# Kernel tuning notes

Measured on AMD Instinct MI355X. Metric: run time of the kernel, lower is better.

Reference implementation:

```python
import jax, jax.numpy as jnp
import numpy as np

EMBED_DIM = 1024
NUM_HEADS = 16
HEAD_DIM = EMBED_DIM // NUM_HEADS


def setup_inputs() -> dict:
    key = jax.random.key(0)
    k1, k2, k3, k4, k5 = jax.random.split(key, 5)
    B, L, C = 4, 4096, EMBED_DIM
    s = 1.0 / np.sqrt(C)
    return {
        "x": jax.random.normal(k1, (B, L, C), dtype=jnp.float32),
        "qkv_w": jax.random.normal(k2, (3 * C, C), dtype=jnp.float32) * s,
        "qkv_b": jax.random.normal(k3, (3 * C,), dtype=jnp.float32) * 0.01,
        "out_w": jax.random.normal(k4, (C, C), dtype=jnp.float32) * s,
        "out_b": jax.random.normal(k5, (C,), dtype=jnp.float32) * 0.01,
        "num_frames": 16,
    }


def reference(x, qkv_w, qkv_b, out_w, out_b, num_frames):
    B, L, C = x.shape
    P = L // num_frames  # patches per frame
    H, D = NUM_HEADS, HEAD_DIM
    xf = x.reshape(B * num_frames, P, C)
    # fused QKV projection (torch Linear: y = x @ W^T + b)
    qkv = xf @ qkv_w.T + qkv_b                      # [BF, P, 3C]
    qkv = qkv.reshape(B * num_frames, P, 3, H, D)
    qkv = jnp.transpose(qkv, (2, 0, 3, 1, 4))        # [3, BF, H, P, D]
    q, k, v = qkv[0], qkv[1], qkv[2]
    scores = jnp.einsum("bhqd,bhkd->bhqk", q, k) / np.sqrt(D)
    attn = jax.nn.softmax(scores, axis=-1)
    out = jnp.einsum("bhqk,bhkd->bhqd", attn, v)     # [BF, H, P, D]
    out = jnp.transpose(out, (0, 2, 1, 3)).reshape(B, L, C)
    return out @ out_w.T + out_b
```

## Files before the change

### kernel.cpp

```cpp
#include <hip/hip_runtime.h>


typedef __bf16 bf16x8 __attribute__((ext_vector_type(8)));
typedef float f32x4 __attribute__((ext_vector_type(4)));

__device__ __forceinline__ void gload_lds16(const void* g, void* l) {
  __builtin_amdgcn_global_load_lds(
      (__attribute__((address_space(1))) void*)(g),
      (__attribute__((address_space(3))) void*)(l), 16, 0, 0);
}

__global__ __launch_bounds__(256) void cvt_f32_bf16(
    const float* __restrict__ in, __bf16* __restrict__ out, int n8) {
  int i = blockIdx.x * 256 + threadIdx.x;
  if (i >= n8) return;
  const float4* p = (const float4*)in;
  float4 a = p[2 * i];
  float4 b = p[2 * i + 1];
  bf16x8 v;
  v[0] = (__bf16)a.x; v[1] = (__bf16)a.y; v[2] = (__bf16)a.z; v[3] = (__bf16)a.w;
  v[4] = (__bf16)b.x; v[5] = (__bf16)b.y; v[6] = (__bf16)b.z; v[7] = (__bf16)b.w;
  ((bf16x8*)out)[i] = v;
}

template <bool BF16_OUT>
__global__ __launch_bounds__(256, 2) void gemm_bt(
    const __bf16* __restrict__ A, const __bf16* __restrict__ Bm,
    const float* __restrict__ bias, void* __restrict__ Cv,
    int M, int N, int K) {
  __shared__ alignas(16) __bf16 As[128 * 32];
  __shared__ alignas(16) __bf16 Bs[128 * 32];

  const int tid = threadIdx.x, lane = tid & 63, wid = tid >> 6;
  const int wm = wid >> 1, wn = wid & 1;
  const int bm = blockIdx.y, bn = blockIdx.x;

  f32x4 acc[4][4] = {};

  const int seg0 = wid * 64 + lane, seg1 = seg0 + 256;
  const __bf16* gA0 = A + (size_t)(bm * 128 + (seg0 >> 2)) * K + (seg0 & 3) * 8;
  const __bf16* gA1 = A + (size_t)(bm * 128 + (seg1 >> 2)) * K + (seg1 & 3) * 8;
  const __bf16* gB0 = Bm + (size_t)(bn * 128 + (seg0 >> 2)) * K + (seg0 & 3) * 8;
  const __bf16* gB1 = Bm + (size_t)(bn * 128 + (seg1 >> 2)) * K + (seg1 & 3) * 8;
  __bf16* lA0 = &As[seg0 * 8];
  __bf16* lA1 = &As[seg1 * 8];
  __bf16* lB0 = &Bs[seg0 * 8];
  __bf16* lB1 = &Bs[seg1 * 8];

  const int ar = lane & 15, kc = (lane >> 4) * 8;
  const __bf16* rA = &As[(wm * 64 + ar) * 32 + kc];
  const __bf16* rB = &Bs[(wn * 64 + ar) * 32 + kc];

  for (int k0 = 0; k0 < K; k0 += 32) {
    gload_lds16(gA0, lA0);
    gload_lds16(gA1, lA1);
    gload_lds16(gB0, lB0);
    gload_lds16(gB1, lB1);
    gA0 += 32; gA1 += 32; gB0 += 32; gB1 += 32;
    __syncthreads();
    bf16x8 av[4], bv[4];
#pragma unroll
    for (int m = 0; m < 4; ++m) av[m] = *(const bf16x8*)(rA + m * 16 * 32);
#pragma unroll
    for (int n = 0; n < 4; ++n) bv[n] = *(const bf16x8*)(rB + n * 16 * 32);
#pragma unroll
    for (int m = 0; m < 4; ++m)
#pragma unroll
      for (int n = 0; n < 4; ++n)
        acc[m][n] = __builtin_amdgcn_mfma_f32_16x16x32_bf16(av[m], bv[n],
                                                            acc[m][n], 0, 0, 0);
    __syncthreads();
  }

  const int r0 = (lane >> 4) * 4, c0 = lane & 15;
#pragma unroll
  for (int m = 0; m < 4; ++m) {
#pragma unroll
    for (int n = 0; n < 4; ++n) {
      int row = bm * 128 + wm * 64 + m * 16 + r0;
      int col = bn * 128 + wn * 64 + n * 16 + c0;
      float bb = bias[col];
#pragma unroll
      for (int r = 0; r < 4; ++r) {
        float v = acc[m][n][r] + bb;
        if (BF16_OUT)
          ((__bf16*)Cv)[(size_t)(row + r) * N + col] = (__bf16)v;
        else
          ((float*)Cv)[(size_t)(row + r) * N + col] = v;
      }
    }
  }
}

__global__ __launch_bounds__(256, 2) void attn_kernel(
    const __bf16* __restrict__ qkv, __bf16* __restrict__ attnOut) {
  __shared__ alignas(16) __bf16 Ks[256 * 64];
  __shared__ alignas(16) __bf16 Vt[64 * 256];
  __shared__ alignas(16) __bf16 Pl[4][64 * 32];

  const int h = blockIdx.x, bf = blockIdx.y;
  const int tid = threadIdx.x, lane = tid & 63, wid = tid >> 6;
  const int l15 = lane & 15, l4 = lane >> 4;

  const __bf16* base = qkv + (size_t)(bf * 256) * 3072 + h * 64;

#pragma unroll
  for (int rr = 0; rr < 8; ++rr) {
    int s = rr * 256 + wid * 64 + lane;
    int r = s >> 3, t = s & 7, c8 = t ^ (r & 7);
    gload_lds16(base + 1024 + (size_t)r * 3072 + c8 * 8, &Ks[s * 8]);
  }

  {
    const __bf16* vrow = base + 2048 + (size_t)tid * 3072;
    bf16x8 vv[8];
#pragma unroll
    for (int b8 = 0; b8 < 8; ++b8) vv[b8] = *(const bf16x8*)(vrow + b8 * 8);
#pragma unroll
    for (int b8 = 0; b8 < 8; ++b8)
#pragma unroll
      for (int e = 0; e < 8; ++e) {
        int d = b8 * 8 + e;
        Vt[d * 256 + (((tid >> 3) ^ (d & 7)) * 8) + (tid & 7)] = vv[b8][e];
      }
  }

  bf16x8 aq[4][2];
  const __bf16* qbase = base + (size_t)(wid * 64) * 3072;
#pragma unroll
  for (int m = 0; m < 4; ++m)
#pragma unroll
    for (int kk = 0; kk < 2; ++kk)
      aq[m][kk] =
          *(const bf16x8*)(qbase + (size_t)(m * 16 + l15) * 3072 + kk * 32 + l4 * 8);

  __syncthreads();

  float m_run[4][4], l_run[4][4];
#pragma unroll
  for (int m = 0; m < 4; ++m)
#pragma unroll
    for (int r = 0; r < 4; ++r) { m_run[m][r] = -3.0e38f; l_run[m][r] = 0.f; }
  f32x4 o[4][4] = {};

  __bf16* Pw = &Pl[wid][0];

  for (int jt = 0; jt < 8; ++jt) {
    f32x4 s[4][2] = {};
#pragma unroll
    for (int kk = 0; kk < 2; ++kk) {
      bf16x8 bk[2];
#pragma unroll
      for (int n = 0; n < 2; ++n) {
        int j = jt * 32 + n * 16 + l15;
        int c8 = kk * 4 + l4;
        bk[n] = *(const bf16x8*)&Ks[(j * 8 + (c8 ^ (j & 7))) * 8];
      }
#pragma unroll
      for (int m = 0; m < 4; ++m)
#pragma unroll
        for (int n = 0; n < 2; ++n)
          s[m][n] = __builtin_amdgcn_mfma_f32_16x16x32_bf16(aq[m][kk], bk[n],
                                                            s[m][n], 0, 0, 0);
    }
#pragma unroll
    for (int m = 0; m < 4; ++m)
#pragma unroll
      for (int r = 0; r < 4; ++r) {
        float a0 = s[m][0][r] * 0.125f, a1 = s[m][1][r] * 0.125f;
        float t = fmaxf(a0, a1);
        t = fmaxf(t, __shfl_xor(t, 1));
        t = fmaxf(t, __shfl_xor(t, 2));
        t = fmaxf(t, __shfl_xor(t, 4));
        t = fmaxf(t, __shfl_xor(t, 8));
        float mn = fmaxf(m_run[m][r], t);
        float al = __expf(m_run[m][r] - mn);
        m_run[m][r] = mn;
        float p0 = __expf(a0 - mn), p1 = __expf(a1 - mn);
        s[m][0][r] = p0; s[m][1][r] = p1;
        float rs = p0 + p1;
        rs += __shfl_xor(rs, 1);
        rs += __shfl_xor(rs, 2);
        rs += __shfl_xor(rs, 4);
        rs += __shfl_xor(rs, 8);
        l_run[m][r] = l_run[m][r] * al + rs;
#pragma unroll
        for (int nd = 0; nd < 4; ++nd) o[m][nd][r] *= al;
      }
#pragma unroll
    for (int m = 0; m < 4; ++m)
#pragma unroll
      for (int n = 0; n < 2; ++n)
#pragma unroll
        for (int r = 0; r < 4; ++r) {
          int q = m * 16 + l4 * 4 + r;
          int j = n * 16 + l15;
          Pw[q * 32 + (((j >> 3) ^ (q & 3)) * 8) + (j & 7)] = (__bf16)s[m][n][r];
        }
    bf16x8 ap[4];
#pragma unroll
    for (int m = 0; m < 4; ++m) {
      int q = m * 16 + l15;
      ap[m] = *(const bf16x8*)&Pw[q * 32 + ((l4 ^ (q & 3)) * 8)];
    }
    bf16x8 bv[4];
#pragma unroll
    for (int nd = 0; nd < 4; ++nd) {
      int d = nd * 16 + l15;
      int jb = jt * 4 + l4;
      bv[nd] = *(const bf16x8*)&Vt[d * 256 + ((jb ^ (d & 7)) * 8)];
    }
#pragma unroll
    for (int m = 0; m < 4; ++m)
#pragma unroll
      for (int nd = 0; nd < 4; ++nd)
        o[m][nd] = __builtin_amdgcn_mfma_f32_16x16x32_bf16(ap[m], bv[nd],
                                                           o[m][nd], 0, 0, 0);
  }

  __bf16* ob = attnOut + (size_t)(bf * 256 + wid * 64) * 1024 + h * 64;
#pragma unroll
  for (int m = 0; m < 4; ++m)
#pragma unroll
    for (int r = 0; r < 4; ++r) {
      float inv = 1.0f / l_run[m][r];
#pragma unroll
      for (int nd = 0; nd < 4; ++nd)
        ob[(size_t)(m * 16 + l4 * 4 + r) * 1024 + nd * 16 + l15] =
            (__bf16)(o[m][nd][r] * inv);
    }
}

extern "C" void kernel_launch(void* const* d_in, const int* in_sizes, int n_in,
                              void* d_out, int out_size, void* d_ws,
                              size_t ws_size, hipStream_t stream) {
  const float* x = (const float*)d_in[0];
  const float* qkv_w = (const float*)d_in[1];
  const float* qkv_b = (const float*)d_in[2];
  const float* out_w = (const float*)d_in[3];
  const float* out_b = (const float*)d_in[4];
  float* out = (float*)d_out;

  __bf16* xb = (__bf16*)d_ws;
  __bf16* qkvwb = xb + 16777216;
  __bf16* outwb = qkvwb + 3145728;
  __bf16* qkvb = outwb + 1048576;
  __bf16* attnb = qkvb + (size_t)16384 * 3072;

  cvt_f32_bf16<<<8192, 256, 0, stream>>>(x, xb, 16777216 / 8);
  cvt_f32_bf16<<<1536, 256, 0, stream>>>(qkv_w, qkvwb, 3145728 / 8);
  cvt_f32_bf16<<<512, 256, 0, stream>>>(out_w, outwb, 1048576 / 8);

  gemm_bt<true><<<dim3(24, 128), 256, 0, stream>>>(xb, qkvwb, qkv_b, qkvb,
                                                   16384, 3072, 1024);

  attn_kernel<<<dim3(16, 64), 256, 0, stream>>>(qkvb, attnb);

  gemm_bt<false><<<dim3(8, 128), 256, 0, stream>>>(attnb, outwb, out_b, out,
                                                   16384, 1024, 1024);
}
```

Baseline: 411.8 us.

## Replace GEMM with 256x256-tile double-buffered LDS kernel and XCD-aware block swizzle

Both projection GEMMs move from a single-buffered 128x128x32 tile with 4 waves to a 256x256x64 tile with 8 waves. Operand tiles are double-buffered in LDS through direct global-to-LDS loads with an XOR swizzle, and fine-grained vmcnt/barrier waits overlap the next tile's loads with MFMA work. Block IDs are remapped across the 8 XCDs, and s_setprio raises priority around the MFMA bursts. The larger tile raises arithmetic intensity, but it uses 128KB of LDS and many accumulator registers, which limits occupancy to one block per CU and leaves fewer blocks for the smaller output GEMM.

```diff
diff --git a/kernel.cpp b/kernel.cpp
--- a/kernel.cpp
+++ b/kernel.cpp
@@ -24,61 +24,154 @@
 }
 
 template <bool BF16_OUT>
-__global__ __launch_bounds__(256, 2) void gemm_bt(
+__global__ __launch_bounds__(512, 2) void gemm256(
     const __bf16* __restrict__ A, const __bf16* __restrict__ Bm,
     const float* __restrict__ bias, void* __restrict__ Cv,
     int M, int N, int K) {
-  __shared__ alignas(16) __bf16 As[128 * 32];
-  __shared__ alignas(16) __bf16 Bs[128 * 32];
+  __shared__ alignas(16) __bf16 Al[2][256 * 64];
+  __shared__ alignas(16) __bf16 Bl[2][256 * 64];
 
   const int tid = threadIdx.x, lane = tid & 63, wid = tid >> 6;
-  const int wm = wid >> 1, wn = wid & 1;
-  const int bm = blockIdx.y, bn = blockIdx.x;
-
-  f32x4 acc[4][4] = {};
-
-  const int seg0 = wid * 64 + lane, seg1 = seg0 + 256;
-  const __bf16* gA0 = A + (size_t)(bm * 128 + (seg0 >> 2)) * K + (seg0 & 3) * 8;
-  const __bf16* gA1 = A + (size_t)(bm * 128 + (seg1 >> 2)) * K + (seg1 & 3) * 8;
-  const __bf16* gB0 = Bm + (size_t)(bn * 128 + (seg0 >> 2)) * K + (seg0 & 3) * 8;
-  const __bf16* gB1 = Bm + (size_t)(bn * 128 + (seg1 >> 2)) * K + (seg1 & 3) * 8;
-  __bf16* lA0 = &As[seg0 * 8];
-  __bf16* lA1 = &As[seg1 * 8];
-  __bf16* lB0 = &Bs[seg0 * 8];
-  __bf16* lB1 = &Bs[seg1 * 8];
-
-  const int ar = lane & 15, kc = (lane >> 4) * 8;
-  const __bf16* rA = &As[(wm * 64 + ar) * 32 + kc];
-  const __bf16* rB = &Bs[(wn * 64 + ar) * 32 + kc];
-
-  for (int k0 = 0; k0 < K; k0 += 32) {
-    gload_lds16(gA0, lA0);
-    gload_lds16(gA1, lA1);
-    gload_lds16(gB0, lB0);
-    gload_lds16(gB1, lB1);
-    gA0 += 32; gA1 += 32; gB0 += 32; gB1 += 32;
-    __syncthreads();
-    bf16x8 av[4], bv[4];
-#pragma unroll
-    for (int m = 0; m < 4; ++m) av[m] = *(const bf16x8*)(rA + m * 16 * 32);
-#pragma unroll
-    for (int n = 0; n < 4; ++n) bv[n] = *(const bf16x8*)(rB + n * 16 * 32);
-#pragma unroll
-    for (int m = 0; m < 4; ++m)
-#pragma unroll
-      for (int n = 0; n < 4; ++n)
-        acc[m][n] = __builtin_amdgcn_mfma_f32_16x16x32_bf16(av[m], bv[n],
-                                                            acc[m][n], 0, 0, 0);
-    __syncthreads();
-  }
-
-  const int r0 = (lane >> 4) * 4, c0 = lane & 15;
-#pragma unroll
-  for (int m = 0; m < 4; ++m) {
-#pragma unroll
-    for (int n = 0; n < 4; ++n) {
-      int row = bm * 128 + wm * 64 + m * 16 + r0;
-      int col = bn * 128 + wn * 64 + n * 16 + c0;
+  const int wr = wid >> 2, wc = wid & 3;
+  const int l15 = lane & 15, l4 = lane >> 4;
+
+  const int nwg = gridDim.x * gridDim.y;
+  const int bid = blockIdx.y * gridDim.x + blockIdx.x;
+  const int q = nwg >> 3;
+  const int swz = (bid & 7) * q + (bid >> 3);
+  const int bn = swz % gridDim.x, bm = swz / gridDim.x;
+
+  const int NT = K >> 6;
+
+  const __bf16* gA[4];
+  const __bf16* gB[4];
+#pragma unroll
+  for (int c = 0; c < 4; ++c) {
+    int seg = c * 512 + tid;
+    int row = seg >> 3, bl = (seg & 7) ^ (row & 7);
+    gA[c] = A + (size_t)(bm * 256 + row) * K + bl * 8;
+    gB[c] = Bm + (size_t)(bn * 256 + row) * K + bl * 8;
+  }
+
+#define STAGE(b)                                         \
+  {                                                      \
+    _Pragma("unroll") for (int c = 0; c < 4; ++c) {      \
+      gload_lds16(gA[c], &Al[b][(c * 512 + tid) * 8]);   \
+      gA[c] += 64;                                       \
+    }                                                    \
+    _Pragma("unroll") for (int c = 0; c < 4; ++c) {      \
+      gload_lds16(gB[c], &Bl[b][(c * 512 + tid) * 8]);   \
+      gB[c] += 64;                                       \
+    }                                                    \
+  }
+
+  const int rsw = l15 & 7;
+  const int pk0 = ((l4) ^ rsw) * 8;
+  const int pk1 = ((4 + l4) ^ rsw) * 8;
+  const int aRow = (wr * 128 + l15) * 64;
+  const int bRow = (wc * 64 + l15) * 64;
+
+  f32x4 acc[8][4] = {};
+
+  STAGE(0);
+  STAGE(1);
+  asm volatile("s_waitcnt vmcnt(8)" ::: "memory");
+  __builtin_amdgcn_s_barrier();
+
+  for (int t = 0; t < NT; ++t) {
+    const __bf16* Ab = &Al[t & 1][0];
+    const __bf16* Bb = &Bl[t & 1][0];
+    const bool hasStage = (t + 2 < NT);
+    const bool hasNext = (t + 1 < NT);
+
+    bf16x8 b0 = *(const bf16x8*)(Bb + bRow + 0 * 1024 + pk0);
+    bf16x8 b1 = *(const bf16x8*)(Bb + bRow + 1 * 1024 + pk0);
+    bf16x8 b2 = *(const bf16x8*)(Bb + bRow + 2 * 1024 + pk0);
+    bf16x8 b3 = *(const bf16x8*)(Bb + bRow + 3 * 1024 + pk0);
+    bf16x8 x0 = *(const bf16x8*)(Ab + aRow + 0 * 1024 + pk0);
+    bf16x8 x1 = *(const bf16x8*)(Ab + aRow + 1 * 1024 + pk0);
+    bf16x8 x2 = *(const bf16x8*)(Ab + aRow + 2 * 1024 + pk0);
+    bf16x8 x3 = *(const bf16x8*)(Ab + aRow + 3 * 1024 + pk0);
+    __builtin_amdgcn_s_setprio(1);
+#pragma unroll
+    for (int n = 0; n < 4; ++n) {
+      bf16x8 bb = n == 0 ? b0 : n == 1 ? b1 : n == 2 ? b2 : b3;
+      acc[0][n] = __builtin_amdgcn_mfma_f32_16x16x32_bf16(x0, bb, acc[0][n], 0, 0, 0);
+      acc[1][n] = __builtin_amdgcn_mfma_f32_16x16x32_bf16(x1, bb, acc[1][n], 0, 0, 0);
+      acc[2][n] = __builtin_amdgcn_mfma_f32_16x16x32_bf16(x2, bb, acc[2][n], 0, 0, 0);
+      acc[3][n] = __builtin_amdgcn_mfma_f32_16x16x32_bf16(x3, bb, acc[3][n], 0, 0, 0);
+    }
+    __builtin_amdgcn_s_setprio(0);
+
+    x0 = *(const bf16x8*)(Ab + aRow + 4 * 1024 + pk0);
+    x1 = *(const bf16x8*)(Ab + aRow + 5 * 1024 + pk0);
+    x2 = *(const bf16x8*)(Ab + aRow + 6 * 1024 + pk0);
+    x3 = *(const bf16x8*)(Ab + aRow + 7 * 1024 + pk0);
+    __builtin_amdgcn_s_setprio(1);
+#pragma unroll
+    for (int n = 0; n < 4; ++n) {
+      bf16x8 bb = n == 0 ? b0 : n == 1 ? b1 : n == 2 ? b2 : b3;
+      acc[4][n] = __builtin_amdgcn_mfma_f32_16x16x32_bf16(x0, bb, acc[4][n], 0, 0, 0);
+      acc[5][n] = __builtin_amdgcn_mfma_f32_16x16x32_bf16(x1, bb, acc[5][n], 0, 0, 0);
+      acc[6][n] = __builtin_amdgcn_mfma_f32_16x16x32_bf16(x2, bb, acc[6][n], 0, 0, 0);
+      acc[7][n] = __builtin_amdgcn_mfma_f32_16x16x32_bf16(x3, bb, acc[7][n], 0, 0, 0);
+    }
+    __builtin_amdgcn_s_setprio(0);
+
+    b0 = *(const bf16x8*)(Bb + bRow + 0 * 1024 + pk1);
+    b1 = *(const bf16x8*)(Bb + bRow + 1 * 1024 + pk1);
+    b2 = *(const bf16x8*)(Bb + bRow + 2 * 1024 + pk1);
+    b3 = *(const bf16x8*)(Bb + bRow + 3 * 1024 + pk1);
+    x0 = *(const bf16x8*)(Ab + aRow + 0 * 1024 + pk1);
+    x1 = *(const bf16x8*)(Ab + aRow + 1 * 1024 + pk1);
+    x2 = *(const bf16x8*)(Ab + aRow + 2 * 1024 + pk1);
+    x3 = *(const bf16x8*)(Ab + aRow + 3 * 1024 + pk1);
+    __builtin_amdgcn_s_setprio(1);
+#pragma unroll
+    for (int n = 0; n < 4; ++n) {
+      bf16x8 bb = n == 0 ? b0 : n == 1 ? b1 : n == 2 ? b2 : b3;
+      acc[0][n] = __builtin_amdgcn_mfma_f32_16x16x32_bf16(x0, bb, acc[0][n], 0, 0, 0);
+      acc[1][n] = __builtin_amdgcn_mfma_f32_16x16x32_bf16(x1, bb, acc[1][n], 0, 0, 0);
+      acc[2][n] = __builtin_amdgcn_mfma_f32_16x16x32_bf16(x2, bb, acc[2][n], 0, 0, 0);
+      acc[3][n] = __builtin_amdgcn_mfma_f32_16x16x32_bf16(x3, bb, acc[3][n], 0, 0, 0);
+    }
+    __builtin_amdgcn_s_setprio(0);
+
+    x0 = *(const bf16x8*)(Ab + aRow + 4 * 1024 + pk1);
+    x1 = *(const bf16x8*)(Ab + aRow + 5 * 1024 + pk1);
+    x2 = *(const bf16x8*)(Ab + aRow + 6 * 1024 + pk1);
+    x3 = *(const bf16x8*)(Ab + aRow + 7 * 1024 + pk1);
+    asm volatile("s_waitcnt lgkmcnt(0)" ::: "memory");
+    __builtin_amdgcn_sched_barrier(0);
+    __builtin_amdgcn_s_barrier();
+    if (hasStage) STAGE(t & 1);
+    __builtin_amdgcn_s_setprio(1);
+#pragma unroll
+    for (int n = 0; n < 4; ++n) {
+      bf16x8 bb = n == 0 ? b0 : n == 1 ? b1 : n == 2 ? b2 : b3;
+      acc[4][n] = __builtin_amdgcn_mfma_f32_16x16x32_bf16(x0, bb, acc[4][n], 0, 0, 0);
+      acc[5][n] = __builtin_amdgcn_mfma_f32_16x16x32_bf16(x1, bb, acc[5][n], 0, 0, 0);
+      acc[6][n] = __builtin_amdgcn_mfma_f32_16x16x32_bf16(x2, bb, acc[6][n], 0, 0, 0);
+      acc[7][n] = __builtin_amdgcn_mfma_f32_16x16x32_bf16(x3, bb, acc[7][n], 0, 0, 0);
+    }
+    __builtin_amdgcn_s_setprio(0);
+    if (hasNext) {
+      if (hasStage)
+        asm volatile("s_waitcnt vmcnt(8)" ::: "memory");
+      else
+        asm volatile("s_waitcnt vmcnt(0)" ::: "memory");
+      __builtin_amdgcn_s_barrier();
+    }
+  }
+#undef STAGE
+
+  const int r0 = l4 * 4;
+#pragma unroll
+  for (int m = 0; m < 8; ++m) {
+#pragma unroll
+    for (int n = 0; n < 4; ++n) {
+      int row = bm * 256 + wr * 128 + m * 16 + r0;
+      int col = bn * 256 + wc * 64 + n * 16 + l15;
       float bb = bias[col];
 #pragma unroll
       for (int r = 0; r < 4; ++r) {
@@ -251,11 +344,11 @@
   cvt_f32_bf16<<<1536, 256, 0, stream>>>(qkv_w, qkvwb, 3145728 / 8);
   cvt_f32_bf16<<<512, 256, 0, stream>>>(out_w, outwb, 1048576 / 8);
 
-  gemm_bt<true><<<dim3(24, 128), 256, 0, stream>>>(xb, qkvwb, qkv_b, qkvb,
-                                                   16384, 3072, 1024);
+  gemm256<true><<<dim3(12, 64), 512, 0, stream>>>(xb, qkvwb, qkv_b, qkvb,
+                                                  16384, 3072, 1024);
 
   attn_kernel<<<dim3(16, 64), 256, 0, stream>>>(qkvb, attnb);
 
-  gemm_bt<false><<<dim3(8, 128), 256, 0, stream>>>(attnb, outwb, out_b, out,
-                                                   16384, 1024, 1024);
-}
+  gemm256<false><<<dim3(4, 64), 512, 0, stream>>>(attnb, outwb, out_b, out,
+                                                  16384, 1024, 1024);
+}
```

New measurement: 379.1 us. -7.9%, faster.

## Replace GEMM with 256x256 tile, multi-buffered LDS pipeline and XCD-aware block swizzle

Applied to the files above, without the earlier changes.

Replaces the 128x128 single-buffered GEMM with a 512-thread 256x256 tile kernel. Global-to-LDS loads for later K-steps are issued ahead of time into four LDS stages, with explicit vmcnt waits, barriers and raised scheduling priority around the MFMA bursts. It also remaps block IDs so neighbouring tiles land on the same XCD for better L2 reuse, and XOR-swizzles the LDS layout to avoid bank conflicts. The aim is to hide load latency and raise MFMA utilisation, at the cost of 128 KB of LDS per block and lower occupancy, with the hand-tuned wait counts fragile if the load pattern changes.

```diff
diff --git a/kernel.cpp b/kernel.cpp
--- a/kernel.cpp
+++ b/kernel.cpp
@@ -9,6 +9,8 @@
       (__attribute__((address_space(1))) void*)(g),
       (__attribute__((address_space(3))) void*)(l), 16, 0, 0);
 }
+
+#define VMW(N) asm volatile("s_waitcnt vmcnt(" #N ")" ::: "memory")
 
 __global__ __launch_bounds__(256) void cvt_f32_bf16(
     const float* __restrict__ in, __bf16* __restrict__ out, int n8) {
@@ -24,61 +26,105 @@
 }
 
 template <bool BF16_OUT>
-__global__ __launch_bounds__(256, 2) void gemm_bt(
+__global__ __launch_bounds__(512, 2) void gemm256(
     const __bf16* __restrict__ A, const __bf16* __restrict__ Bm,
     const float* __restrict__ bias, void* __restrict__ Cv,
     int M, int N, int K) {
-  __shared__ alignas(16) __bf16 As[128 * 32];
-  __shared__ alignas(16) __bf16 Bs[128 * 32];
+  __shared__ alignas(16) __bf16 Asl[2][2][256 * 32];
+  __shared__ alignas(16) __bf16 Bsl[2][2][256 * 32];
 
   const int tid = threadIdx.x, lane = tid & 63, wid = tid >> 6;
-  const int wm = wid >> 1, wn = wid & 1;
-  const int bm = blockIdx.y, bn = blockIdx.x;
-
-  f32x4 acc[4][4] = {};
-
-  const int seg0 = wid * 64 + lane, seg1 = seg0 + 256;
-  const __bf16* gA0 = A + (size_t)(bm * 128 + (seg0 >> 2)) * K + (seg0 & 3) * 8;
-  const __bf16* gA1 = A + (size_t)(bm * 128 + (seg1 >> 2)) * K + (seg1 & 3) * 8;
-  const __bf16* gB0 = Bm + (size_t)(bn * 128 + (seg0 >> 2)) * K + (seg0 & 3) * 8;
-  const __bf16* gB1 = Bm + (size_t)(bn * 128 + (seg1 >> 2)) * K + (seg1 & 3) * 8;
-  __bf16* lA0 = &As[seg0 * 8];
-  __bf16* lA1 = &As[seg1 * 8];
-  __bf16* lB0 = &Bs[seg0 * 8];
-  __bf16* lB1 = &Bs[seg1 * 8];
-
-  const int ar = lane & 15, kc = (lane >> 4) * 8;
-  const __bf16* rA = &As[(wm * 64 + ar) * 32 + kc];
-  const __bf16* rB = &Bs[(wn * 64 + ar) * 32 + kc];
-
-  for (int k0 = 0; k0 < K; k0 += 32) {
-    gload_lds16(gA0, lA0);
-    gload_lds16(gA1, lA1);
-    gload_lds16(gB0, lB0);
-    gload_lds16(gB1, lB1);
-    gA0 += 32; gA1 += 32; gB0 += 32; gB1 += 32;
-    __syncthreads();
-    bf16x8 av[4], bv[4];
-#pragma unroll
-    for (int m = 0; m < 4; ++m) av[m] = *(const bf16x8*)(rA + m * 16 * 32);
-#pragma unroll
-    for (int n = 0; n < 4; ++n) bv[n] = *(const bf16x8*)(rB + n * 16 * 32);
-#pragma unroll
-    for (int m = 0; m < 4; ++m)
-#pragma unroll
-      for (int n = 0; n < 4; ++n)
-        acc[m][n] = __builtin_amdgcn_mfma_f32_16x16x32_bf16(av[m], bv[n],
-                                                            acc[m][n], 0, 0, 0);
-    __syncthreads();
-  }
-
-  const int r0 = (lane >> 4) * 4, c0 = lane & 15;
-#pragma unroll
-  for (int m = 0; m < 4; ++m) {
+  const int wr = wid >> 2, wc = wid & 3;
+  const int l15 = lane & 15, l4 = lane >> 4;
+
+  const int nwg = gridDim.x * gridDim.y;
+  const int bid = blockIdx.y * gridDim.x + blockIdx.x;
+  const int swz = (bid & 7) * (nwg >> 3) + (bid >> 3);
+  const int bn = swz % gridDim.x, bm = swz / gridDim.x;
+
+  const int NT = K >> 6;
+
+  const int srow = tid >> 2;
+  const int sblk = (tid & 3) ^ ((srow >> 2) & 3);
+  const __bf16* sA = A + (size_t)(bm * 256 + srow) * K + sblk * 8;
+  const __bf16* sB = Bm + (size_t)(bn * 256 + srow) * K + sblk * 8;
+  const size_t rs128 = (size_t)128 * K;
+
+#define STG(MATP, DST, kOff)                              \
+  {                                                       \
+    gload_lds16(MATP + (kOff), &(DST)[tid * 8]);          \
+    gload_lds16(MATP + rs128 + (kOff), &(DST)[4096 + tid * 8]); \
+  }
+
+  const int pk = ((l4 ^ (l15 >> 2)) & 3) * 8;
+  const int raOff = (wr * 128 + l15) * 32 + pk;
+  const int rbOff = (wc * 64 + l15) * 32 + pk;
+
+  f32x4 acc[8][4] = {};
+  bf16x8 a_[8];
+  bf16x8 b_[4];
+
+#define PH(BUF, KK, CH, STAGE_STMT, GATE_STMT)                        \
+  {                                                                   \
+    const __bf16* Ab = &Asl[BUF][KK][0];                              \
+    const __bf16* Bb = &Bsl[BUF][KK][0];                              \
+    if (CH == 0) {                                                    \
+      _Pragma("unroll") for (int m = 0; m < 8; ++m)                   \
+          a_[m] = *(const bf16x8*)(Ab + raOff + m * 512);             \
+    }                                                                 \
+    b_[CH * 2 + 0] = *(const bf16x8*)(Bb + rbOff + (CH * 2 + 0) * 512); \
+    b_[CH * 2 + 1] = *(const bf16x8*)(Bb + rbOff + (CH * 2 + 1) * 512); \
+    STAGE_STMT;                                                       \
+    __builtin_amdgcn_s_barrier();                                     \
+    asm volatile("s_waitcnt lgkmcnt(0)" ::: "memory");                \
+    __builtin_amdgcn_sched_barrier(0);                                \
+    __builtin_amdgcn_s_setprio(1);                                    \
+    _Pragma("unroll") for (int m = 0; m < 8; ++m) {                   \
+      acc[m][CH * 2 + 0] = __builtin_amdgcn_mfma_f32_16x16x32_bf16(   \
+          a_[m], b_[CH * 2 + 0], acc[m][CH * 2 + 0], 0, 0, 0);        \
+      acc[m][CH * 2 + 1] = __builtin_amdgcn_mfma_f32_16x16x32_bf16(   \
+          a_[m], b_[CH * 2 + 1], acc[m][CH * 2 + 1], 0, 0, 0);        \
+    }                                                                 \
+    __builtin_amdgcn_s_setprio(0);                                    \
+    GATE_STMT;                                                        \
+    __builtin_amdgcn_s_barrier();                                     \
+  }
+
+  STG(sA, Asl[0][0], 0);
+  STG(sB, Bsl[0][0], 0);
+  STG(sA, Asl[0][1], 32);
+  STG(sB, Bsl[0][1], 32);
+  STG(sA, Asl[1][0], 64);
+  STG(sB, Bsl[1][0], 64);
+  STG(sA, Asl[1][1], 96);
+  VMW(10);
+  __builtin_amdgcn_s_barrier();
+
+  for (int t = 0; t < NT; t += 2) {
+    const bool st2 = (t + 2 < NT);
+    PH(0, 0, 0, { STG(sB, Bsl[1][1], (t + 1) * 64 + 32); }, {});
+    PH(0, 0, 1, { if (st2) STG(sA, Asl[0][0], (t + 2) * 64); },
+       { if (st2) VMW(10); else VMW(8); });
+    PH(0, 1, 0, { if (st2) STG(sB, Bsl[0][0], (t + 2) * 64); }, {});
+    PH(0, 1, 1, { if (st2) STG(sA, Asl[0][1], (t + 2) * 64 + 32); },
+       { if (st2) VMW(10); else VMW(4); });
+    PH(1, 0, 0, { if (st2) STG(sB, Bsl[0][1], (t + 2) * 64 + 32); }, {});
+    PH(1, 0, 1, { if (st2) STG(sA, Asl[1][0], (t + 3) * 64); },
+       { if (st2) VMW(10); else VMW(0); });
+    PH(1, 1, 0, { if (st2) STG(sB, Bsl[1][0], (t + 3) * 64); }, {});
+    PH(1, 1, 1, { if (st2) STG(sA, Asl[1][1], (t + 3) * 64 + 32); },
+       { if (st2) VMW(10); });
+  }
+#undef PH
+#undef STG
+
+  const int r0 = l4 * 4;
+#pragma unroll
+  for (int m = 0; m < 8; ++m) {
 #pragma unroll
     for (int n = 0; n < 4; ++n) {
-      int row = bm * 128 + wm * 64 + m * 16 + r0;
-      int col = bn * 128 + wn * 64 + n * 16 + c0;
+      int row = bm * 256 + wr * 128 + m * 16 + r0;
+      int col = bn * 256 + wc * 64 + n * 16 + l15;
       float bb = bias[col];
 #pragma unroll
       for (int r = 0; r < 4; ++r) {
@@ -251,11 +297,11 @@
   cvt_f32_bf16<<<1536, 256, 0, stream>>>(qkv_w, qkvwb, 3145728 / 8);
   cvt_f32_bf16<<<512, 256, 0, stream>>>(out_w, outwb, 1048576 / 8);
 
-  gemm_bt<true><<<dim3(24, 128), 256, 0, stream>>>(xb, qkvwb, qkv_b, qkvb,
-                                                   16384, 3072, 1024);
+  gemm256<true><<<dim3(12, 64), 512, 0, stream>>>(xb, qkvwb, qkv_b, qkvb,
+                                                  16384, 3072, 1024);
 
   attn_kernel<<<dim3(16, 64), 256, 0, stream>>>(qkvb, attnb);
 
-  gemm_bt<false><<<dim3(8, 128), 256, 0, stream>>>(attnb, outwb, out_b, out,
-                                                   16384, 1024, 1024);
-}
+  gemm256<false><<<dim3(4, 64), 512, 0, stream>>>(attnb, outwb, out_b, out,
+                                                  16384, 1024, 1024);
+}
```

New measurement: 396.7 us. -3.7%, faster.
